# Optimization experiments

Measured on AMD Instinct MI355X. Metric: run time of the kernel, lower is better.

Reference implementation:

```python
import jax, jax.numpy as jnp
import numpy as np

TAU = 18.0


def smooth_compose(X, M, tau=TAU):
    # Z[n,i,j] = smooth_min(X[n,i], M[i,j]) = -(1/tau) * log(exp(-tau*X) + exp(-tau*M))
    # Y[n,j]   = (1/tau) * logsumexp(tau * Z[n,:,j], axis over i)
    # tau*Z = -logaddexp(-tau*X, -tau*M)  (numerically stable, same math)
    tZ = -jnp.logaddexp(-tau * X[:, :, None], -tau * M[None, :, :])  # [n, d, d]
    return (1.0 / tau) * jax.nn.logsumexp(tZ, axis=1)  # [n, d]


def setup_inputs() -> dict:
    key = jax.random.key(0)
    k1, k2, k3, k4, k5 = jax.random.split(key, 5)
    n, p, d = 2048, 1024, 256
    S = jax.random.uniform(k1, (n, p), dtype=jnp.float32)
    T = jax.random.uniform(k2, (n, p), dtype=jnp.float32)
    # learned parameters (A0/M0/B0 defaults are 0.5-filled; use random values of similar scale)
    A = jax.random.uniform(k3, (p, d), dtype=jnp.float32)
    # rawM = logit(M0); random small logits -> M = sigmoid(rawM) near 0.5
    rawM = 0.5 * jax.random.normal(k4, (d, d), dtype=jnp.float32)
    B = jax.random.uniform(k5, (d, p), dtype=jnp.float32)
    return {"S": S, "T": T, "A": A, "rawM": rawM, "B": B}


def reference(S, T, A, rawM, B):
    M = jax.nn.sigmoid(rawM)            # [d, d]
    X_hat = S @ A                       # [n, d]
    Y_hat = T @ A                       # [n, d]
    X_box = jnp.clip(X_hat, 0.0, 1.0)
    Y_box = jnp.clip(Y_hat, 0.0, 1.0)
    Y_pred = smooth_compose(X_box, M, tau=TAU)  # [n, d]
    S_rec = X_hat @ B                   # [n, p]
    T_rec = Y_hat @ B                   # [n, p]
    T_pred = Y_pred @ B                 # [n, p]
    return (X_hat, Y_hat, X_box, Y_box, Y_pred, S_rec, T_rec, T_pred)
```

## Files before the change

### kernel.cpp

```cpp
#include <hip/hip_runtime.h>
#include <math.h>

constexpr int N = 2048;
constexpr int P = 1024;
constexpr int D = 256;
constexpr float TAU = 18.0f;

constexpr size_t OFF_XHAT  = 0;
constexpr size_t OFF_YHAT  = (size_t)N * D;
constexpr size_t OFF_XBOX  = 2 * (size_t)N * D;
constexpr size_t OFF_YBOX  = 3 * (size_t)N * D;
constexpr size_t OFF_YPRED = 4 * (size_t)N * D;
constexpr size_t OFF_SREC  = 5 * (size_t)N * D;

constexpr size_t WS_ATH = 0;
constexpr size_t WS_ATL = 524288;
constexpr size_t WS_BTH = 1048576;
constexpr size_t WS_BTL = 1572864;
constexpr size_t WS_V   = 2097152;
constexpr size_t WS_U   = 2359296;
constexpr size_t WS_LHH = 4456448;
constexpr size_t WS_LHL = 7602176;

typedef short bhalf8 __attribute__((ext_vector_type(8)));
typedef float f32x4  __attribute__((ext_vector_type(4)));

__device__ inline short f2bf(float f) {
  union { float f; unsigned u; } x; x.f = f;
  unsigned r = (x.u + 0x7FFFu + ((x.u >> 16) & 1u)) >> 16;
  return (short)r;
}
__device__ inline float bf2f(short h) {
  union { unsigned u; float f; } x; x.u = ((unsigned)(unsigned short)h) << 16;
  return x.f;
}

__device__ inline void transpose_hilo_body(
    const float* __restrict__ src, short* __restrict__ dh,
    short* __restrict__ dl, int R, int C, int bx, int by, int t) {
  __shared__ __align__(16) float tile[32][36];
  const int r0 = bx * 32, c0 = by * 32;
  {
    const int tr = t >> 3, tc4 = (t & 7) * 4;
    float4 x = *(const float4*)(src + (size_t)(r0 + tr) * C + c0 + tc4);
    *(float4*)&tile[tr][tc4] = x;
  }
  __syncthreads();
  {
    const int tc = t >> 3, tr4 = (t & 7) * 4;
    short4 h, l;
    float f0 = tile[tr4 + 0][tc];
    float f1 = tile[tr4 + 1][tc];
    float f2 = tile[tr4 + 2][tc];
    float f3 = tile[tr4 + 3][tc];
    h.x = f2bf(f0); l.x = f2bf(f0 - bf2f(h.x));
    h.y = f2bf(f1); l.y = f2bf(f1 - bf2f(h.y));
    h.z = f2bf(f2); l.z = f2bf(f2 - bf2f(h.z));
    h.w = f2bf(f3); l.w = f2bf(f3 - bf2f(h.w));
    *(short4*)(dh + (size_t)(c0 + tc) * R + r0 + tr4) = h;
    *(short4*)(dl + (size_t)(c0 + tc) * R + r0 + tr4) = l;
  }
}

__global__ __launch_bounds__(256) void prep_all_kernel(
    const float* __restrict__ A, const float* __restrict__ rawM,
    const float* __restrict__ B, short* __restrict__ Ath,
    short* __restrict__ Atl, short* __restrict__ Bth,
    short* __restrict__ Btl, float* __restrict__ V) {
  const int bid = blockIdx.x;
  const int t = threadIdx.x;
  if (bid < 64) {
    const int idx = (bid * 256 + t) * 4;
    float4 x = *(const float4*)(rawM + idx);
    float4 o;
    o.x = expf(-TAU / (1.0f + expf(-x.x)));
    o.y = expf(-TAU / (1.0f + expf(-x.y)));
    o.z = expf(-TAU / (1.0f + expf(-x.z)));
    o.w = expf(-TAU / (1.0f + expf(-x.w)));
    *(float4*)(V + idx) = o;
  } else if (bid < 320) {
    const int idx = bid - 64;
    transpose_hilo_body(A, Ath, Atl, P, D, idx & 31, idx >> 5, t);
  } else {
    const int idx = bid - 320;
    transpose_hilo_body(B, Bth, Btl, D, P, idx & 7, idx >> 3, t);
  }
}

__global__ __launch_bounds__(256) void gemm1_mfma(
    const float* __restrict__ S, const float* __restrict__ Tm,
    const short* __restrict__ Ath, const short* __restrict__ Atl,
    float* __restrict__ out, float* __restrict__ U,
    short* __restrict__ LHh, short* __restrict__ LHl) {
  __shared__ __align__(16) short As_h[2][32][40];
  __shared__ __align__(16) short As_l[2][32][40];
  __shared__ __align__(16) short Bs_h[2][64][40];
  __shared__ __align__(16) short Bs_l[2][64][40];

  const int t  = threadIdx.x;
  const int m0 = blockIdx.x * 32, n0 = blockIdx.y * 64;

  const int arow = t >> 3;
  const int ak   = (t & 7) * 4;
  const int grow = m0 + arow;
  const float* Lrow = (grow < N) ? (S + (size_t)grow * P)
                                 : (Tm + (size_t)(grow - N) * P);
  const int brow = t >> 2;
  const int bk   = (t & 3) * 8;
  const short* BhR = Ath + (size_t)(n0 + brow) * P;
  const short* BlR = Atl + (size_t)(n0 + brow) * P;

  const int l = t & 63, w = t >> 6;
  const int wr = (w & 1) * 16, wc = (w >> 1) * 32;
  const int fr = l & 15, ko8 = (l >> 4) * 8, rq = (l >> 4) * 4;

  f32x4 acc[2];
  acc[0] = (f32x4){0.f, 0.f, 0.f, 0.f};
  acc[1] = (f32x4){0.f, 0.f, 0.f, 0.f};

  float4 pa  = *(const float4*)(Lrow + ak);
  bhalf8 pbh = *(const bhalf8*)(BhR + bk);
  bhalf8 pbl = *(const bhalf8*)(BlR + bk);

#define STAGE1(buf)                                        \
  do {                                                     \
    short4 ah4, al4;                                       \
    ah4.x = f2bf(pa.x); al4.x = f2bf(pa.x - bf2f(ah4.x));  \
    ah4.y = f2bf(pa.y); al4.y = f2bf(pa.y - bf2f(ah4.y));  \
    ah4.z = f2bf(pa.z); al4.z = f2bf(pa.z - bf2f(ah4.z));  \
    ah4.w = f2bf(pa.w); al4.w = f2bf(pa.w - bf2f(ah4.w));  \
    *(short4*)&As_h[buf][arow][ak] = ah4;                  \
    *(short4*)&As_l[buf][arow][ak] = al4;                  \
    *(bhalf8*)&Bs_h[buf][brow][bk] = pbh;                  \
    *(bhalf8*)&Bs_l[buf][brow][bk] = pbl;                  \
  } while (0)

  STAGE1(0);

  for (int ks = 0; ks < 32; ++ks) {
    const int b = ks & 1;
    if (ks < 31) {
      const int kn = (ks + 1) * 32;
      pa  = *(const float4*)(Lrow + kn + ak);
      pbh = *(const bhalf8*)(BhR + kn + bk);
      pbl = *(const bhalf8*)(BlR + kn + bk);
    }
    __syncthreads();
    bhalf8 ahv = *(const bhalf8*)&As_h[b][wr + fr][ko8];
    bhalf8 alv = *(const bhalf8*)&As_l[b][wr + fr][ko8];
#pragma unroll
    for (int ni = 0; ni < 2; ++ni) {
      bhalf8 bhv = *(const bhalf8*)&Bs_h[b][wc + ni * 16 + fr][ko8];
      bhalf8 blv = *(const bhalf8*)&Bs_l[b][wc + ni * 16 + fr][ko8];
      acc[ni] = __builtin_amdgcn_mfma_f32_16x16x32_bf16(ahv, bhv, acc[ni], 0, 0, 0);
      acc[ni] = __builtin_amdgcn_mfma_f32_16x16x32_bf16(ahv, blv, acc[ni], 0, 0, 0);
      acc[ni] = __builtin_amdgcn_mfma_f32_16x16x32_bf16(alv, bhv, acc[ni], 0, 0, 0);
    }
    if (ks < 31) STAGE1((ks + 1) & 1);
  }
#undef STAGE1

#pragma unroll
  for (int ni = 0; ni < 2; ++ni) {
    const int col = n0 + wc + ni * 16 + fr;
#pragma unroll
    for (int r = 0; r < 4; ++r) {
      const int row = m0 + wr + rq + r;
      const float v = acc[ni][r];
      const float c = fminf(fmaxf(v, 0.0f), 1.0f);
      const short h  = f2bf(v);
      const short lo = f2bf(v - bf2f(h));
      LHh[(size_t)row * D + col] = h;
      LHl[(size_t)row * D + col] = lo;
      if (row < N) {
        out[OFF_XHAT + (size_t)row * D + col] = v;
        out[OFF_XBOX + (size_t)row * D + col] = c;
        U[(size_t)row * D + col] = expf(-TAU * c);
      } else {
        const size_t ry = (size_t)(row - N);
        out[OFF_YHAT + ry * D + col] = v;
        out[OFF_YBOX + ry * D + col] = c;
      }
    }
  }
}

__global__ __launch_bounds__(256) void smooth_kernel(
    const float* __restrict__ U, const float* __restrict__ V,
    float* __restrict__ ypred, short* __restrict__ LHh,
    short* __restrict__ LHl) {
  __shared__ float us[256][17];
  const int t = threadIdx.x;
  const int n0 = blockIdx.x * 16, j0 = blockIdx.y * 32;

  {
    const int sr = t & 15;
    const int si = (t >> 4) * 16;
    const float* up = U + (size_t)(n0 + sr) * D + si;
#pragma unroll
    for (int q = 0; q < 16; q += 4) {
      float4 x = *(const float4*)(up + q);
      us[si + q + 0][sr] = x.x;
      us[si + q + 1][sr] = x.y;
      us[si + q + 2][sr] = x.z;
      us[si + q + 3][sr] = x.w;
    }
  }
  __syncthreads();

  const int jg = (t & 15) * 2;
  const int nn = t >> 4;
  const float* vp = V + j0 + jg;

  float acc0 = 0.f, acc1 = 0.f;
#pragma unroll 8
  for (int i = 0; i < D; ++i) {
    const float u = us[i][nn];
    float2 v2 = *(const float2*)(vp + (size_t)i * D);
    acc0 += __builtin_amdgcn_rcpf(u + v2.x);
    acc1 += __builtin_amdgcn_rcpf(u + v2.y);
  }

  const int row = n0 + nn;
  float2 o;
  o.x = (1.0f / TAU) * logf(acc0);
  o.y = (1.0f / TAU) * logf(acc1);
  *(float2*)(ypred + (size_t)row * D + j0 + jg) = o;
  short2 h2, l2;
  h2.x = f2bf(o.x); l2.x = f2bf(o.x - bf2f(h2.x));
  h2.y = f2bf(o.y); l2.y = f2bf(o.y - bf2f(h2.y));
  const size_t lrow = (size_t)(2 * N + row) * D + j0 + jg;
  *(short2*)(LHh + lrow) = h2;
  *(short2*)(LHl + lrow) = l2;
}

__global__ __launch_bounds__(256) void gemm2_mfma(
    const short* __restrict__ LHh, const short* __restrict__ LHl,
    const short* __restrict__ Bth, const short* __restrict__ Btl,
    float* __restrict__ rec) {
  __shared__ __align__(16) short As_h[2][64][40];
  __shared__ __align__(16) short As_l[2][64][40];
  __shared__ __align__(16) short Bs_h[2][64][40];
  __shared__ __align__(16) short Bs_l[2][64][40];

  const int t  = threadIdx.x;
  const int m0 = blockIdx.x * 64, n0 = blockIdx.y * 64;

  const int srow = t >> 2;
  const int sk   = (t & 3) * 8;
  const short* AhR = LHh + (size_t)(m0 + srow) * D;
  const short* AlR = LHl + (size_t)(m0 + srow) * D;
  const short* BhR = Bth + (size_t)(n0 + srow) * D;
  const short* BlR = Btl + (size_t)(n0 + srow) * D;

  const int l = t & 63, w = t >> 6;
  const int wr = (w & 1) * 32, wc = (w >> 1) * 32;
  const int fr = l & 15, ko8 = (l >> 4) * 8, rq = (l >> 4) * 4;

  f32x4 acc[2][2];
#pragma unroll
  for (int i = 0; i < 2; ++i)
#pragma unroll
    for (int j = 0; j < 2; ++j) acc[i][j] = (f32x4){0.f, 0.f, 0.f, 0.f};

  bhalf8 pah = *(const bhalf8*)(AhR + sk);
  bhalf8 pal = *(const bhalf8*)(AlR + sk);
  bhalf8 pbh = *(const bhalf8*)(BhR + sk);
  bhalf8 pbl = *(const bhalf8*)(BlR + sk);

#define STAGE2(buf)                            \
  do {                                         \
    *(bhalf8*)&As_h[buf][srow][sk] = pah;      \
    *(bhalf8*)&As_l[buf][srow][sk] = pal;      \
    *(bhalf8*)&Bs_h[buf][srow][sk] = pbh;      \
    *(bhalf8*)&Bs_l[buf][srow][sk] = pbl;      \
  } while (0)

  STAGE2(0);

  for (int ks = 0; ks < 8; ++ks) {
    const int b = ks & 1;
    if (ks < 7) {
      const int kn = (ks + 1) * 32;
      pah = *(const bhalf8*)(AhR + kn + sk);
      pal = *(const bhalf8*)(AlR + kn + sk);
      pbh = *(const bhalf8*)(BhR + kn + sk);
      pbl = *(const bhalf8*)(BlR + kn + sk);
    }
    __syncthreads();
    bhalf8 ahv[2], alv[2], bhv[2], blv[2];
#pragma unroll
    for (int mi = 0; mi < 2; ++mi) {
      ahv[mi] = *(const bhalf8*)&As_h[b][wr + mi * 16 + fr][ko8];
      alv[mi] = *(const bhalf8*)&As_l[b][wr + mi * 16 + fr][ko8];
      bhv[mi] = *(const bhalf8*)&Bs_h[b][wc + mi * 16 + fr][ko8];
      blv[mi] = *(const bhalf8*)&Bs_l[b][wc + mi * 16 + fr][ko8];
    }
#pragma unroll
    for (int mi = 0; mi < 2; ++mi)
#pragma unroll
      for (int ni = 0; ni < 2; ++ni) {
        acc[mi][ni] = __builtin_amdgcn_mfma_f32_16x16x32_bf16(ahv[mi], bhv[ni], acc[mi][ni], 0, 0, 0);
        acc[mi][ni] = __builtin_amdgcn_mfma_f32_16x16x32_bf16(ahv[mi], blv[ni], acc[mi][ni], 0, 0, 0);
        acc[mi][ni] = __builtin_amdgcn_mfma_f32_16x16x32_bf16(alv[mi], bhv[ni], acc[mi][ni], 0, 0, 0);
      }
    if (ks < 7) STAGE2((ks + 1) & 1);
  }
#undef STAGE2

#pragma unroll
  for (int mi = 0; mi < 2; ++mi)
#pragma unroll
    for (int ni = 0; ni < 2; ++ni) {
      const int col = n0 + wc + ni * 16 + fr;
#pragma unroll
      for (int r = 0; r < 4; ++r) {
        const int row = m0 + wr + mi * 16 + rq + r;
        rec[(size_t)row * P + col] = acc[mi][ni][r];
      }
    }
}

extern "C" void kernel_launch(void* const* d_in, const int* in_sizes, int n_in,
                              void* d_out, int out_size, void* d_ws,
                              size_t ws_size, hipStream_t stream) {
  const float* S    = (const float*)d_in[0];
  const float* T    = (const float*)d_in[1];
  const float* A    = (const float*)d_in[2];
  const float* rawM = (const float*)d_in[3];
  const float* B    = (const float*)d_in[4];
  float* out = (float*)d_out;
  char* ws = (char*)d_ws;

  short* Ath = (short*)(ws + WS_ATH);
  short* Atl = (short*)(ws + WS_ATL);
  short* Bth = (short*)(ws + WS_BTH);
  short* Btl = (short*)(ws + WS_BTL);
  float* V   = (float*)(ws + WS_V);
  float* U   = (float*)(ws + WS_U);
  short* LHh = (short*)(ws + WS_LHH);
  short* LHl = (short*)(ws + WS_LHL);

  prep_all_kernel<<<576, 256, 0, stream>>>(A, rawM, B, Ath, Atl, Bth, Btl, V);
  gemm1_mfma<<<dim3(128, 4), 256, 0, stream>>>(S, T, Ath, Atl, out, U, LHh, LHl);
  smooth_kernel<<<dim3(128, 8), 256, 0, stream>>>(U, V, out + OFF_YPRED, LHh, LHl);
  gemm2_mfma<<<dim3(96, 16), 256, 0, stream>>>(LHh, LHl, Bth, Btl, out + OFF_SREC);
}
```

Baseline: 148.3 us.

## Pre-split S/T to bf16 hi/lo, enlarge K tiles, XCD swizzle, retile smooth and gemm2

```diff
diff --git a/kernel.cpp b/kernel.cpp
--- a/kernel.cpp
+++ b/kernel.cpp
@@ -21,6 +21,8 @@
 constexpr size_t WS_U   = 2359296;
 constexpr size_t WS_LHH = 4456448;
 constexpr size_t WS_LHL = 7602176;
+constexpr size_t WS_STH = 10747904;
+constexpr size_t WS_STL = 19136512;
 
 typedef short bhalf8 __attribute__((ext_vector_type(8)));
 typedef float f32x4  __attribute__((ext_vector_type(4)));
@@ -33,6 +35,10 @@
 __device__ inline float bf2f(short h) {
   union { unsigned u; float f; } x; x.u = ((unsigned)(unsigned short)h) << 16;
   return x.f;
+}
+__device__ inline int xcd_swz(int bid, int nwg) {
+  const int cpx = nwg >> 3;
+  return (bid & 7) * cpx + (bid >> 3);
 }
 
 __device__ inline void transpose_hilo_body(
@@ -63,10 +69,12 @@
 }
 
 __global__ __launch_bounds__(256) void prep_all_kernel(
+    const float* __restrict__ S, const float* __restrict__ Tm,
     const float* __restrict__ A, const float* __restrict__ rawM,
     const float* __restrict__ B, short* __restrict__ Ath,
     short* __restrict__ Atl, short* __restrict__ Bth,
-    short* __restrict__ Btl, float* __restrict__ V) {
+    short* __restrict__ Btl, float* __restrict__ V,
+    short* __restrict__ STh, short* __restrict__ STl) {
   const int bid = blockIdx.x;
   const int t = threadIdx.x;
   if (bid < 64) {
@@ -81,32 +89,48 @@
   } else if (bid < 320) {
     const int idx = bid - 64;
     transpose_hilo_body(A, Ath, Atl, P, D, idx & 31, idx >> 5, t);
-  } else {
+  } else if (bid < 576) {
     const int idx = bid - 320;
     transpose_hilo_body(B, Bth, Btl, D, P, idx & 7, idx >> 3, t);
+  } else {
+    const int idx = bid - 576;
+#pragma unroll
+    for (int q = 0; q < 4; ++q) {
+      const int row = idx * 4 + q;
+      const float* src = (row < N) ? (S + (size_t)row * P)
+                                   : (Tm + (size_t)(row - N) * P);
+      float4 x = *(const float4*)(src + t * 4);
+      short4 h, l;
+      h.x = f2bf(x.x); l.x = f2bf(x.x - bf2f(h.x));
+      h.y = f2bf(x.y); l.y = f2bf(x.y - bf2f(h.y));
+      h.z = f2bf(x.z); l.z = f2bf(x.z - bf2f(h.z));
+      h.w = f2bf(x.w); l.w = f2bf(x.w - bf2f(h.w));
+      *(short4*)(STh + (size_t)row * P + t * 4) = h;
+      *(short4*)(STl + (size_t)row * P + t * 4) = l;
+    }
   }
 }
 
 __global__ __launch_bounds__(256) void gemm1_mfma(
-    const float* __restrict__ S, const float* __restrict__ Tm,
+    const short* __restrict__ STh, const short* __restrict__ STl,
     const short* __restrict__ Ath, const short* __restrict__ Atl,
     float* __restrict__ out, float* __restrict__ U,
     short* __restrict__ LHh, short* __restrict__ LHl) {
-  __shared__ __align__(16) short As_h[2][32][40];
-  __shared__ __align__(16) short As_l[2][32][40];
-  __shared__ __align__(16) short Bs_h[2][64][40];
-  __shared__ __align__(16) short Bs_l[2][64][40];
+  __shared__ __align__(16) short As_h[2][32][72];
+  __shared__ __align__(16) short As_l[2][32][72];
+  __shared__ __align__(16) short Bs_h[2][64][72];
+  __shared__ __align__(16) short Bs_l[2][64][72];
 
   const int t  = threadIdx.x;
-  const int m0 = blockIdx.x * 32, n0 = blockIdx.y * 64;
+  const int wg = xcd_swz(blockIdx.x, 512);
+  const int m0 = (wg >> 2) * 32, n0 = (wg & 3) * 64;
 
   const int arow = t >> 3;
-  const int ak   = (t & 7) * 4;
-  const int grow = m0 + arow;
-  const float* Lrow = (grow < N) ? (S + (size_t)grow * P)
-                                 : (Tm + (size_t)(grow - N) * P);
+  const int ak   = (t & 7) * 8;
+  const short* AhR = STh + (size_t)(m0 + arow) * P;
+  const short* AlR = STl + (size_t)(m0 + arow) * P;
   const int brow = t >> 2;
-  const int bk   = (t & 3) * 8;
+  const int bk   = (t & 3) * 16;
   const short* BhR = Ath + (size_t)(n0 + brow) * P;
   const short* BlR = Atl + (size_t)(n0 + brow) * P;
 
@@ -118,45 +142,53 @@
   acc[0] = (f32x4){0.f, 0.f, 0.f, 0.f};
   acc[1] = (f32x4){0.f, 0.f, 0.f, 0.f};
 
-  float4 pa  = *(const float4*)(Lrow + ak);
-  bhalf8 pbh = *(const bhalf8*)(BhR + bk);
-  bhalf8 pbl = *(const bhalf8*)(BlR + bk);
-
-#define STAGE1(buf)                                        \
-  do {                                                     \
-    short4 ah4, al4;                                       \
-    ah4.x = f2bf(pa.x); al4.x = f2bf(pa.x - bf2f(ah4.x));  \
-    ah4.y = f2bf(pa.y); al4.y = f2bf(pa.y - bf2f(ah4.y));  \
-    ah4.z = f2bf(pa.z); al4.z = f2bf(pa.z - bf2f(ah4.z));  \
-    ah4.w = f2bf(pa.w); al4.w = f2bf(pa.w - bf2f(ah4.w));  \
-    *(short4*)&As_h[buf][arow][ak] = ah4;                  \
-    *(short4*)&As_l[buf][arow][ak] = al4;                  \
-    *(bhalf8*)&Bs_h[buf][brow][bk] = pbh;                  \
-    *(bhalf8*)&Bs_l[buf][brow][bk] = pbl;                  \
+  bhalf8 pah, pal, pbh0, pbh1, pbl0, pbl1;
+  pah  = *(const bhalf8*)(AhR + ak);
+  pal  = *(const bhalf8*)(AlR + ak);
+  pbh0 = *(const bhalf8*)(BhR + bk);
+  pbh1 = *(const bhalf8*)(BhR + bk + 8);
+  pbl0 = *(const bhalf8*)(BlR + bk);
+  pbl1 = *(const bhalf8*)(BlR + bk + 8);
+
+#define STAGE1(buf)                                   \
+  do {                                                \
+    *(bhalf8*)&As_h[buf][arow][ak]    = pah;          \
+    *(bhalf8*)&As_l[buf][arow][ak]    = pal;          \
+    *(bhalf8*)&Bs_h[buf][brow][bk]    = pbh0;         \
+    *(bhalf8*)&Bs_h[buf][brow][bk+8]  = pbh1;         \
+    *(bhalf8*)&Bs_l[buf][brow][bk]    = pbl0;         \
+    *(bhalf8*)&Bs_l[buf][brow][bk+8]  = pbl1;         \
   } while (0)
 
   STAGE1(0);
 
-  for (int ks = 0; ks < 32; ++ks) {
+  for (int ks = 0; ks < 16; ++ks) {
     const int b = ks & 1;
-    if (ks < 31) {
-      const int kn = (ks + 1) * 32;
-      pa  = *(const float4*)(Lrow + kn + ak);
-      pbh = *(const bhalf8*)(BhR + kn + bk);
-      pbl = *(const bhalf8*)(BlR + kn + bk);
+    if (ks < 15) {
+      const int kn = (ks + 1) * 64;
+      pah  = *(const bhalf8*)(AhR + kn + ak);
+      pal  = *(const bhalf8*)(AlR + kn + ak);
+      pbh0 = *(const bhalf8*)(BhR + kn + bk);
+      pbh1 = *(const bhalf8*)(BhR + kn + bk + 8);
+      pbl0 = *(const bhalf8*)(BlR + kn + bk);
+      pbl1 = *(const bhalf8*)(BlR + kn + bk + 8);
     }
     __syncthreads();
-    bhalf8 ahv = *(const bhalf8*)&As_h[b][wr + fr][ko8];
-    bhalf8 alv = *(const bhalf8*)&As_l[b][wr + fr][ko8];
-#pragma unroll
-    for (int ni = 0; ni < 2; ++ni) {
-      bhalf8 bhv = *(const bhalf8*)&Bs_h[b][wc + ni * 16 + fr][ko8];
-      bhalf8 blv = *(const bhalf8*)&Bs_l[b][wc + ni * 16 + fr][ko8];
-      acc[ni] = __builtin_amdgcn_mfma_f32_16x16x32_bf16(ahv, bhv, acc[ni], 0, 0, 0);
-      acc[ni] = __builtin_amdgcn_mfma_f32_16x16x32_bf16(ahv, blv, acc[ni], 0, 0, 0);
-      acc[ni] = __builtin_amdgcn_mfma_f32_16x16x32_bf16(alv, bhv, acc[ni], 0, 0, 0);
-    }
-    if (ks < 31) STAGE1((ks + 1) & 1);
+#pragma unroll
+    for (int ks2 = 0; ks2 < 2; ++ks2) {
+      const int ko = ks2 * 32 + ko8;
+      bhalf8 ahv = *(const bhalf8*)&As_h[b][wr + fr][ko];
+      bhalf8 alv = *(const bhalf8*)&As_l[b][wr + fr][ko];
+#pragma unroll
+      for (int ni = 0; ni < 2; ++ni) {
+        bhalf8 bhv = *(const bhalf8*)&Bs_h[b][wc + ni * 16 + fr][ko];
+        bhalf8 blv = *(const bhalf8*)&Bs_l[b][wc + ni * 16 + fr][ko];
+        acc[ni] = __builtin_amdgcn_mfma_f32_16x16x32_bf16(ahv, bhv, acc[ni], 0, 0, 0);
+        acc[ni] = __builtin_amdgcn_mfma_f32_16x16x32_bf16(ahv, blv, acc[ni], 0, 0, 0);
+        acc[ni] = __builtin_amdgcn_mfma_f32_16x16x32_bf16(alv, bhv, acc[ni], 0, 0, 0);
+      }
+    }
+    if (ks < 15) STAGE1((ks + 1) & 1);
   }
 #undef STAGE1
 
@@ -189,16 +221,16 @@
     const float* __restrict__ U, const float* __restrict__ V,
     float* __restrict__ ypred, short* __restrict__ LHh,
     short* __restrict__ LHl) {
-  __shared__ float us[256][17];
+  __shared__ float us[256][34];
   const int t = threadIdx.x;
-  const int n0 = blockIdx.x * 16, j0 = blockIdx.y * 32;
+  const int n0 = blockIdx.x * 32, j0 = blockIdx.y * 32;
 
   {
-    const int sr = t & 15;
-    const int si = (t >> 4) * 16;
+    const int sr = t & 31;
+    const int si = (t >> 5) * 32;
     const float* up = U + (size_t)(n0 + sr) * D + si;
 #pragma unroll
-    for (int q = 0; q < 16; q += 4) {
+    for (int q = 0; q < 32; q += 4) {
       float4 x = *(const float4*)(up + q);
       us[si + q + 0][sr] = x.x;
       us[si + q + 1][sr] = x.y;
@@ -209,52 +241,61 @@
   __syncthreads();
 
   const int jg = (t & 15) * 2;
-  const int nn = t >> 4;
+  const int nn = (t >> 4) * 2;
   const float* vp = V + j0 + jg;
 
-  float acc0 = 0.f, acc1 = 0.f;
+  float acc00 = 0.f, acc01 = 0.f, acc10 = 0.f, acc11 = 0.f;
 #pragma unroll 8
   for (int i = 0; i < D; ++i) {
-    const float u = us[i][nn];
+    float2 u2 = *(const float2*)&us[i][nn];
     float2 v2 = *(const float2*)(vp + (size_t)i * D);
-    acc0 += __builtin_amdgcn_rcpf(u + v2.x);
-    acc1 += __builtin_amdgcn_rcpf(u + v2.y);
-  }
-
-  const int row = n0 + nn;
-  float2 o;
-  o.x = (1.0f / TAU) * logf(acc0);
-  o.y = (1.0f / TAU) * logf(acc1);
-  *(float2*)(ypred + (size_t)row * D + j0 + jg) = o;
-  short2 h2, l2;
-  h2.x = f2bf(o.x); l2.x = f2bf(o.x - bf2f(h2.x));
-  h2.y = f2bf(o.y); l2.y = f2bf(o.y - bf2f(h2.y));
-  const size_t lrow = (size_t)(2 * N + row) * D + j0 + jg;
-  *(short2*)(LHh + lrow) = h2;
-  *(short2*)(LHl + lrow) = l2;
-}
-
-__global__ __launch_bounds__(256) void gemm2_mfma(
+    acc00 += __builtin_amdgcn_rcpf(u2.x + v2.x);
+    acc01 += __builtin_amdgcn_rcpf(u2.x + v2.y);
+    acc10 += __builtin_amdgcn_rcpf(u2.y + v2.x);
+    acc11 += __builtin_amdgcn_rcpf(u2.y + v2.y);
+  }
+
+  float a[2][2] = {{acc00, acc01}, {acc10, acc11}};
+#pragma unroll
+  for (int pI = 0; pI < 2; ++pI) {
+    const int row = n0 + nn + pI;
+    float2 o;
+    o.x = (1.0f / TAU) * logf(a[pI][0]);
+    o.y = (1.0f / TAU) * logf(a[pI][1]);
+    *(float2*)(ypred + (size_t)row * D + j0 + jg) = o;
+    short2 h2, l2;
+    h2.x = f2bf(o.x); l2.x = f2bf(o.x - bf2f(h2.x));
+    h2.y = f2bf(o.y); l2.y = f2bf(o.y - bf2f(h2.y));
+    const size_t lrow = (size_t)(2 * N + row) * D + j0 + jg;
+    *(short2*)(LHh + lrow) = h2;
+    *(short2*)(LHl + lrow) = l2;
+  }
+}
+
+__global__ __launch_bounds__(512) void gemm2_mfma(
     const short* __restrict__ LHh, const short* __restrict__ LHl,
     const short* __restrict__ Bth, const short* __restrict__ Btl,
     float* __restrict__ rec) {
-  __shared__ __align__(16) short As_h[2][64][40];
-  __shared__ __align__(16) short As_l[2][64][40];
+  __shared__ __align__(16) short As_h[2][128][40];
+  __shared__ __align__(16) short As_l[2][128][40];
   __shared__ __align__(16) short Bs_h[2][64][40];
   __shared__ __align__(16) short Bs_l[2][64][40];
 
   const int t  = threadIdx.x;
-  const int m0 = blockIdx.x * 64, n0 = blockIdx.y * 64;
-
-  const int srow = t >> 2;
-  const int sk   = (t & 3) * 8;
-  const short* AhR = LHh + (size_t)(m0 + srow) * D;
-  const short* AlR = LHl + (size_t)(m0 + srow) * D;
-  const short* BhR = Bth + (size_t)(n0 + srow) * D;
-  const short* BlR = Btl + (size_t)(n0 + srow) * D;
+  const int wg = xcd_swz(blockIdx.x, 768);
+  const int m0 = (wg >> 4) * 128, n0 = (wg & 15) * 64;
+
+  const int arow = t >> 2;
+  const int ak   = (t & 3) * 8;
+  const short* AhR = LHh + (size_t)(m0 + arow) * D;
+  const short* AlR = LHl + (size_t)(m0 + arow) * D;
+  const int brow = t >> 3;
+  const int bk   = (t & 7) * 4;
+  const short* BhR = Bth + (size_t)(n0 + brow) * D;
+  const short* BlR = Btl + (size_t)(n0 + brow) * D;
 
   const int l = t & 63, w = t >> 6;
-  const int wr = (w & 1) * 32, wc = (w >> 1) * 32;
+  const int wr = (w & 3) * 32, wc = (w >> 2) * 32;
   const int fr = l & 15, ko8 = (l >> 4) * 8, rq = (l >> 4) * 4;
 
   f32x4 acc[2][2];
@@ -263,17 +304,19 @@
 #pragma unroll
     for (int j = 0; j < 2; ++j) acc[i][j] = (f32x4){0.f, 0.f, 0.f, 0.f};
 
-  bhalf8 pah = *(const bhalf8*)(AhR + sk);
-  bhalf8 pal = *(const bhalf8*)(AlR + sk);
-  bhalf8 pbh = *(const bhalf8*)(BhR + sk);
-  bhalf8 pbl = *(const bhalf8*)(BlR + sk);
+  bhalf8 pah, pal;
+  short4 pbh, pbl;
+  pah = *(const bhalf8*)(AhR + ak);
+  pal = *(const bhalf8*)(AlR + ak);
+  pbh = *(const short4*)(BhR + bk);
+  pbl = *(const short4*)(BlR + bk);
 
 #define STAGE2(buf)                            \
   do {                                         \
-    *(bhalf8*)&As_h[buf][srow][sk] = pah;      \
-    *(bhalf8*)&As_l[buf][srow][sk] = pal;      \
-    *(bhalf8*)&Bs_h[buf][srow][sk] = pbh;      \
-    *(bhalf8*)&Bs_l[buf][srow][sk] = pbl;      \
+    *(bhalf8*)&As_h[buf][arow][ak] = pah;      \
+    *(bhalf8*)&As_l[buf][arow][ak] = pal;      \
+    *(short4*)&Bs_h[buf][brow][bk] = pbh;      \
+    *(short4*)&Bs_l[buf][brow][bk] = pbl;      \
   } while (0)
 
   STAGE2(0);
@@ -282,10 +325,10 @@
     const int b = ks & 1;
     if (ks < 7) {
       const int kn = (ks + 1) * 32;
-      pah = *(const bhalf8*)(AhR + kn + sk);
-      pal = *(const bhalf8*)(AlR + kn + sk);
-      pbh = *(const bhalf8*)(BhR + kn + sk);
-      pbl = *(const bhalf8*)(BlR + kn + sk);
+      pah = *(const bhalf8*)(AhR + kn + ak);
+      pal = *(const bhalf8*)(AlR + kn + ak);
+      pbh = *(const short4*)(BhR + kn + bk);
+      pbl = *(const short4*)(BlR + kn + bk);
     }
     __syncthreads();
     bhalf8 ahv[2], alv[2], bhv[2], blv[2];
@@ -340,9 +383,13 @@
   float* U   = (float*)(ws + WS_U);
   short* LHh = (short*)(ws + WS_LHH);
   short* LHl = (short*)(ws + WS_LHL);
-
-  prep_all_kernel<<<576, 256, 0, stream>>>(A, rawM, B, Ath, Atl, Bth, Btl, V);
-  gemm1_mfma<<<dim3(128, 4), 256, 0, stream>>>(S, T, Ath, Atl, out, U, LHh, LHl);
-  smooth_kernel<<<dim3(128, 8), 256, 0, stream>>>(U, V, out + OFF_YPRED, LHh, LHl);
-  gemm2_mfma<<<dim3(96, 16), 256, 0, stream>>>(LHh, LHl, Bth, Btl, out + OFF_SREC);
-}
+  short* STh = (short*)(ws + WS_STH);
+  short* STl = (short*)(ws + WS_STL);
+
+  prep_all_kernel<<<1600, 256, 0, stream>>>(S, T, A, rawM, B, Ath, Atl, Bth,
+                                            Btl, V, STh, STl);
+  gemm1_mfma<<<512, 256, 0, stream>>>(STh, STl, Ath, Atl, out, U, LHh, LHl);
+  smooth_kernel<<<dim3(64, 8), 256, 0, stream>>>(U, V, out + OFF_YPRED, LHh,
+                                                 LHl);
+  gemm2_mfma<<<768, 512, 0, stream>>>(LHh, LHl, Bth, Btl, out + OFF_SREC);
+}
```

Result: faster. 133.7 us (-9.9%).
